# Performance work log

Hardware: AMD Instinct MI355X
Metric: run time of the kernel (lower is better)

Reference implementation:

```python
import jax, jax.numpy as jnp
import numpy as np
import math

B, N, D, H, T = 256, 512, 512, 8, 128
HD = D // H
CLIP = 10.0
CAP = 1.0
NEG = -1.0e9


def setup_inputs() -> dict:
    key = jax.random.key(0)
    ks = jax.random.split(key, 12)
    s = 1.0 / math.sqrt(D)
    return {
        "embeddings": jax.random.normal(ks[0], (B, N, D), jnp.float32),
        "mean_graph_emb": jax.random.normal(ks[1], (B, D), jnp.float32),
        "used_capacity": jax.random.uniform(ks[2], (T, B), jnp.float32),
        "Wk": jax.random.normal(ks[3], (D, D), jnp.float32) * s,
        "Wk_tanh": jax.random.normal(ks[4], (D, D), jnp.float32) * s,
        "Wv": jax.random.normal(ks[5], (D, D), jnp.float32) * s,
        "Wq_context": jax.random.normal(ks[6], (D, D), jnp.float32) * s,
        "Wq_step": jax.random.normal(ks[7], (D + 1, D), jnp.float32) * s,
        "Wout": jax.random.normal(ks[8], (D, D), jnp.float32) * s,
        "prev_a": jax.random.randint(ks[9], (T, B), 0, N, jnp.int32),
        "mask": jax.random.randint(ks[10], (T, B, N), 0, 2, jnp.int32),
    }


def reference(embeddings, mean_graph_emb, used_capacity, Wk, Wk_tanh, Wv,
              Wq_context, Wq_step, Wout, prev_a, mask):
    # Projections (done once per graph embedding, as in get_projections)
    K = (embeddings @ Wk).reshape(B, N, H, HD).transpose(0, 2, 1, 3)      # [B,H,N,hd]
    V = (embeddings @ Wv).reshape(B, N, H, HD).transpose(0, 2, 1, 3)      # [B,H,N,hd]
    K_tanh = embeddings @ Wk_tanh                                          # [B,N,D]
    Q_context = mean_graph_emb @ Wq_context                                # [B,D]

    inv_sqrt_hd = 1.0 / math.sqrt(HD)
    inv_sqrt_d = 1.0 / math.sqrt(D)

    def step(carry, xs):
        prev_t, cap_t, mask_t = xs  # [B], [B], [B,N]
        # get_step_context: gather prev node embedding + remaining capacity
        cur_emb = jnp.take_along_axis(embeddings, prev_t[:, None, None], axis=1)[:, 0]  # [B,D]
        step_ctx = jnp.concatenate([cur_emb, (CAP - cap_t)[:, None]], axis=-1)          # [B,D+1]
        q = Q_context + step_ctx @ Wq_step                                               # [B,D]
        qh = q.reshape(B, H, HD)                                                          # [B,H,hd]
        # decoder MHA, seq_len_q = 1
        logits = jnp.einsum("bhd,bhnd->bhn", qh, K) * inv_sqrt_hd                        # [B,H,N]
        logits = jnp.where(mask_t[:, None, :] == 1, NEG, logits)
        attn = jax.nn.softmax(logits, axis=-1)
        mha = jnp.einsum("bhn,bhnd->bhd", attn, V).reshape(B, D) @ Wout                  # [B,D]
        # single-head tanh-clipped pointer logits
        comp = jnp.einsum("bd,bnd->bn", mha, K_tanh) * inv_sqrt_d                        # [B,N]
        comp = jnp.tanh(comp) * CLIP
        comp = jnp.where(mask_t == 1, NEG, comp)
        p = jax.nn.softmax(comp, axis=-1)                                                # [B,N]
        return carry, p

    _, ps = jax.lax.scan(step, None, (prev_a, used_capacity, mask))  # [T,B,N]
    return ps.transpose(1, 0, 2)  # [B,T,N]
```

## Files before the change

kernel.cpp:

```cpp
#include <hip/hip_runtime.h>
#include <hip/hip_bf16.h>

constexpr int Bb = 256;
constexpr int Nn = 512;
constexpr int Dd = 512;
constexpr int Hh = 8;
constexpr int Tt = 128;
#define NEGF (-1.0e9f)

typedef __attribute__((ext_vector_type(4))) float f32x4;
typedef __attribute__((ext_vector_type(8))) short bf16x8;
typedef __attribute__((ext_vector_type(8))) unsigned short u16x8;

#define AS1 __attribute__((address_space(1)))
#define AS3 __attribute__((address_space(3)))

__device__ __forceinline__ unsigned short f2bf(float f) {
  union { float f; unsigned u; } v; v.f = f;
  unsigned r = v.u + 0x7fffu + ((v.u >> 16) & 1u);
  return (unsigned short)(r >> 16);
}

__device__ __forceinline__ unsigned cvtpk(float lo, float hi) {
  unsigned r;
  asm("v_cvt_pk_bf16_f32 %0, %1, %2" : "=v"(r) : "v"(lo), "v"(hi));
  return r;
}

__global__ void cast_emb_k(const float* __restrict__ src, unsigned short* __restrict__ dst, int n8) {
  int i = blockIdx.x * 256 + threadIdx.x;
  if (i >= n8) return;
  const float4* s = (const float4*)src + (size_t)i * 2;
  float4 a = s[0], b = s[1];
  u16x8 o;
  o[0] = f2bf(a.x); o[1] = f2bf(a.y); o[2] = f2bf(a.z); o[3] = f2bf(a.w);
  o[4] = f2bf(b.x); o[5] = f2bf(b.y); o[6] = f2bf(b.z); o[7] = f2bf(b.w);
  ((u16x8*)dst)[i] = o;
}

__global__ void cast_wt_k(const float* __restrict__ W0, const float* __restrict__ W1,
                          const float* __restrict__ W2,
                          unsigned short* __restrict__ D0, unsigned short* __restrict__ D1,
                          unsigned short* __restrict__ D2) {
  int mid = blockIdx.x >> 8;
  int tile = blockIdx.x & 255;
  const float* S = (mid == 0) ? W0 : (mid == 1) ? W1 : W2;
  unsigned short* Dst = (mid == 0) ? D0 : (mid == 1) ? D1 : D2;
  __shared__ float t[32][33];
  int r0 = (tile >> 4) * 32, c0 = (tile & 15) * 32;
  int tx = threadIdx.x & 31, ty = threadIdx.x >> 5;
#pragma unroll
  for (int yy = 0; yy < 4; ++yy) {
    int r = ty + yy * 8;
    t[r][tx] = S[(size_t)(r0 + r) * 512 + c0 + tx];
  }
  __syncthreads();
#pragma unroll
  for (int yy = 0; yy < 4; ++yy) {
    int c = ty + yy * 8;
    Dst[(size_t)(c0 + c) * 512 + r0 + tx] = f2bf(t[tx][c]);
  }
}

__global__ void qc_k(const float* __restrict__ mge, const float* __restrict__ Wqc,
                     float* __restrict__ Qc) {
  int b = blockIdx.x;
  __shared__ float m[512];
  m[threadIdx.x] = mge[(size_t)b * 512 + threadIdx.x];
  m[threadIdx.x + 256] = mge[(size_t)b * 512 + threadIdx.x + 256];
  __syncthreads();
  float a0 = 0.f, a1 = 0.f;
  for (int k = 0; k < 512; ++k) {
    float mk = m[k];
    a0 += mk * Wqc[(size_t)k * 512 + threadIdx.x];
    a1 += mk * Wqc[(size_t)k * 512 + threadIdx.x + 256];
  }
  Qc[(size_t)b * 512 + threadIdx.x] = a0;
  Qc[(size_t)b * 512 + threadIdx.x + 256] = a1;
}

__global__ void gather_k(const unsigned short* __restrict__ embB, const int* __restrict__ prev,
                         unsigned short* __restrict__ SC) {
  int row = blockIdx.x * 4 + (threadIdx.x >> 6);
  int lane = threadIdx.x & 63;
  int t = row >> 8, b = row & 255;
  int pa = prev[t * Bb + b];
  const u16x8* s = (const u16x8*)(embB + (size_t)(b * 512 + pa) * 512) + lane;
  *((u16x8*)(SC + (size_t)row * 512) + lane) = *s;
}

__global__ void mbits_k(const int* __restrict__ mask, unsigned* __restrict__ bits) {
  size_t gid = (size_t)blockIdx.x * 256 + threadIdx.x;
  int mv = mask[gid];
  unsigned long long bal = __ballot(mv == 1);
  if ((threadIdx.x & 63) == 0) {
    unsigned t = (unsigned)(gid >> 17);
    unsigned b = (unsigned)((gid >> 9) & 255);
    unsigned n = (unsigned)(gid & 511);
    unsigned* dst = bits + (((size_t)b * 128 + t) * 16 + (n >> 5));
    dst[0] = (unsigned)bal;
    dst[1] = (unsigned)(bal >> 32);
  }
}

__device__ __forceinline__ void stage_tile(const unsigned short* __restrict__ G, int row0, int k0,
                                           unsigned short* lds_base, int wave, int lane) {
#pragma unroll
  for (int c = 0; c < 4; ++c) {
    int chunk = wave * 4 + c;
    const unsigned short* g = G + (size_t)(row0 + chunk * 8 + (lane >> 3)) * 512 + k0 + (lane & 7) * 8;
    __builtin_amdgcn_global_load_lds((AS1 void*)g, (AS3 void*)(lds_base + chunk * 512), 16, 0, 0);
  }
}

template <int MODE>
__global__ __launch_bounds__(256, 2)
void gemm5_k(const unsigned short* __restrict__ A, const unsigned short* __restrict__ BT,
             void* __restrict__ Cout,
             const float* __restrict__ Qc, const float* __restrict__ WqsL,
             const float* __restrict__ capp) {
  __shared__ __align__(16) char lds[32768];
  unsigned short* ldsA = (unsigned short*)lds;
  unsigned short* ldsB = ldsA + 8192;
  int xcd = blockIdx.x & 7, loc = blockIdx.x >> 3;
  int ml = loc >> 2, nt = loc & 3;
  int mt = xcd * 32 + ml;
  int m0 = mt * 128, n0 = nt * 128;
  int tid = threadIdx.x, lane = tid & 63, w = tid >> 6;
  int wm = w >> 1, wn = w & 1;
  int l15 = lane & 15, l4 = lane >> 4;

  f32x4 acc[4][4] = {};
  for (int k0 = 0; k0 < 512; k0 += 64) {
    stage_tile(A, m0, k0, ldsA, w, lane);
    stage_tile(BT, n0, k0, ldsB, w, lane);
    __syncthreads();
#pragma unroll
    for (int ks = 0; ks < 2; ++ks) {
      bf16x8 fa[4], fb[4];
#pragma unroll
      for (int ii = 0; ii < 4; ++ii)
        fa[ii] = *(const bf16x8*)(ldsA + (wm * 64 + ii * 16 + l15) * 64 + ks * 32 + l4 * 8);
#pragma unroll
      for (int jj = 0; jj < 4; ++jj)
        fb[jj] = *(const bf16x8*)(ldsB + (wn * 64 + jj * 16 + l15) * 64 + ks * 32 + l4 * 8);
#pragma unroll
      for (int ii = 0; ii < 4; ++ii)
#pragma unroll
        for (int jj = 0; jj < 4; ++jj)
          acc[ii][jj] = __builtin_amdgcn_mfma_f32_16x16x32_bf16(fa[ii], fb[jj], acc[ii][jj], 0, 0, 0);
    }
    __syncthreads();
  }

  if (MODE == 1) {
    unsigned short* C = (unsigned short*)Cout;
#pragma unroll
    for (int ii = 0; ii < 4; ++ii)
#pragma unroll
      for (int jj = 0; jj < 4; ++jj)
#pragma unroll
        for (int r = 0; r < 4; ++r) {
          int row = m0 + wm * 64 + ii * 16 + l4 * 4 + r;
          int col = n0 + wn * 64 + jj * 16 + l15;
          C[(size_t)row * 512 + col] = f2bf(acc[ii][jj][r]);
        }
  } else {
    unsigned short* C = (unsigned short*)Cout;
#pragma unroll
    for (int ii = 0; ii < 4; ++ii)
#pragma unroll
      for (int jj = 0; jj < 4; ++jj)
#pragma unroll
        for (int r = 0; r < 4; ++r) {
          int row = m0 + wm * 64 + ii * 16 + l4 * 4 + r;
          int col = n0 + wn * 64 + jj * 16 + l15;
          int t = row >> 8, bbx = row & 255;
          float val = acc[ii][jj][r] + Qc[(size_t)bbx * 512 + col] + (1.0f - capp[row]) * WqsL[col];
          C[(size_t)(bbx * 128 + t) * 512 + col] = f2bf(val * 0.125f);
        }
  }
}

__global__ __launch_bounds__(256, 2)
void wf_k(const unsigned short* __restrict__ A, const unsigned short* __restrict__ BT,
          unsigned short* __restrict__ C) {
  __shared__ __align__(16) char lds[32768];
  unsigned short* ldsA = (unsigned short*)lds;
  unsigned short* ldsB = ldsA + 8192;
  int mt = blockIdx.x >> 2, nt = blockIdx.x & 3;
  int m0 = mt * 128, n0 = nt * 128;
  int tid = threadIdx.x, lane = tid & 63, w = tid >> 6;
  int wm = w >> 1, wn = w & 1;
  int l15 = lane & 15, l4 = lane >> 4;

  f32x4 acc[4][4] = {};
  for (int k0 = 0; k0 < 512; k0 += 64) {
    stage_tile(A, m0, k0, ldsA, w, lane);
    stage_tile(BT, n0, k0, ldsB, w, lane);
    __syncthreads();
#pragma unroll
    for (int ks = 0; ks < 2; ++ks) {
      bf16x8 fa[4], fb[4];
#pragma unroll
      for (int ii = 0; ii < 4; ++ii)
        fa[ii] = *(const bf16x8*)(ldsA + (wm * 64 + ii * 16 + l15) * 64 + ks * 32 + l4 * 8);
#pragma unroll
      for (int jj = 0; jj < 4; ++jj)
        fb[jj] = *(const bf16x8*)(ldsB + (wn * 64 + jj * 16 + l15) * 64 + ks * 32 + l4 * 8);
#pragma unroll
      for (int ii = 0; ii < 4; ++ii)
#pragma unroll
        for (int jj = 0; jj < 4; ++jj)
          acc[ii][jj] = __builtin_amdgcn_mfma_f32_16x16x32_bf16(fa[ii], fb[jj], acc[ii][jj], 0, 0, 0);
    }
    __syncthreads();
  }
#pragma unroll
  for (int ii = 0; ii < 4; ++ii)
#pragma unroll
    for (int jj = 0; jj < 4; ++jj)
#pragma unroll
      for (int r = 0; r < 4; ++r) {
        int row = m0 + wm * 64 + ii * 16 + l4 * 4 + r;
        int col = n0 + wn * 64 + jj * 16 + l15;
        C[(size_t)row * 512 + col] = f2bf(acc[ii][jj][r]);
      }
}

#define STAGE8(SLOT, MAT, H, KT)                                                   \
  do {                                                                             \
    const unsigned short* G_ = (MAT) ? BT : A;                                     \
    int rb_ = ((MAT) ? n0 : m0) + (H) * 128;                                       \
    char* Lb_ = lds + (SLOT) * 65536 + (MAT) * 32768 + (H) * 16384;                \
    _Pragma("unroll")                                                              \
    for (int sh_ = 0; sh_ < 2; ++sh_) {                                            \
      int off_ = sh_ * 8192 + tid * 16;                                            \
      int r_ = off_ >> 7;                                                          \
      int c_ = (off_ & 127) ^ ((r_ & 7) << 4);     \
      const char* g_ = (const char*)(G_ + (size_t)(rb_ + r_) * 512 + (KT) * 64) + c_; \
      __builtin_amdgcn_global_load_lds((AS1 void*)g_, (AS3 void*)(Lb_ + off_), 16, 0, 0); \
    }                                                                              \
  } while (0)

#define LDA_Q(QM)                                                   \
  _Pragma("unroll")                                                 \
  for (int ii = 0; ii < 4; ++ii) {                                  \
    int rr_ = (QM) * 64 + ii * 16 + l15;                            \
    const char* ap_ = ldsAh + rr_ * 128;                            \
    int sw_ = (rr_ & 7) << 4;                                       \
    fa[ii][0] = *(const bf16x8*)(ap_ + ((l4 * 16) ^ sw_));          \
    fa[ii][1] = *(const bf16x8*)(ap_ + ((64 + l4 * 16) ^ sw_));     \
  }

#define LDB_Q(QN)                                                   \
  _Pragma("unroll")                                                 \
  for (int jj = 0; jj < 2; ++jj) {                                  \
    int rr_ = (wn & 1) * 64 + (QN) * 32 + jj * 16 + l15;            \
    const char* bp_ = ldsBh + rr_ * 128;                            \
    int sw_ = (rr_ & 7) << 4;                                       \
    fb[jj][0] = *(const bf16x8*)(bp_ + ((l4 * 16) ^ sw_));          \
    fb[jj][1] = *(const bf16x8*)(bp_ + ((64 + l4 * 16) ^ sw_));     \
  }

#define MM16(QM, QN)                                                              \
  do {                                                                            \
    __builtin_amdgcn_s_setprio(1);                                                \
    _Pragma("unroll")                                                             \
    for (int ii = 0; ii < 4; ++ii)                                                \
      _Pragma("unroll")                                                           \
      for (int jj = 0; jj < 2; ++jj) {                                            \
        acc[(QM) * 4 + ii][(QN) * 2 + jj] = __builtin_amdgcn_mfma_f32_16x16x32_bf16( \
            fa[ii][0], fb[jj][0], acc[(QM) * 4 + ii][(QN) * 2 + jj], 0, 0, 0);    \
        acc[(QM) * 4 + ii][(QN) * 2 + jj] = __builtin_amdgcn_mfma_f32_16x16x32_bf16( \
            fa[ii][1], fb[jj][1], acc[(QM) * 4 + ii][(QN) * 2 + jj], 0, 0, 0);    \
      }                                                                           \
    __builtin_amdgcn_s_setprio(0);                                                \
  } while (0)

__global__ __launch_bounds__(512, 1)
void gemm8f_k(const unsigned short* __restrict__ A,
              const unsigned short* __restrict__ B0, const unsigned short* __restrict__ B1,
              unsigned short* __restrict__ C0, unsigned short* __restrict__ C2) {
  __shared__ __align__(16) char lds[131072];
  int xcd = blockIdx.x & 7, loc = blockIdx.x >> 3;
  int ml = loc >> 2, cmb = loc & 3;
  int grp = cmb >> 1, nh = cmb & 1;
  const unsigned short* BT = grp ? B1 : B0;
  int mt = xcd * 64 + ml;
  int m0 = mt * 256;
  int n0 = nh * 256;
  int tid = threadIdx.x, lane = tid & 63, w = tid >> 6;
  int wm = w >> 2, wn = w & 3;
  int l15 = lane & 15, l4 = lane >> 4;

  f32x4 acc[8][4] = {};
  bf16x8 fa[4][2], fb[2][2];

  STAGE8(0, 0, 0, 0); STAGE8(0, 0, 1, 0); STAGE8(0, 1, 0, 0); STAGE8(0, 1, 1, 0);

  for (int kt = 0; kt < 8; ++kt) {
    int s = kt & 1, sn = s ^ 1;
    char* ldsAh = lds + s * 65536 + wm * 16384;
    char* ldsBh = lds + s * 65536 + 32768 + (wn >> 1) * 16384;
    if (kt < 7) {
      STAGE8(sn, 0, 0, kt + 1);
      asm volatile("s_waitcnt vmcnt(2)" ::: "memory");
    } else {
      asm volatile("s_waitcnt vmcnt(0)" ::: "memory");
    }
    __builtin_amdgcn_s_barrier();
    LDA_Q(0); LDB_Q(0);
    MM16(0, 0);
    __builtin_amdgcn_s_barrier();
    LDB_Q(1);
    if (kt < 7) STAGE8(sn, 0, 1, kt + 1);
    __builtin_amdgcn_s_barrier();
    MM16(0, 1);
    __builtin_amdgcn_s_barrier();
    LDA_Q(1);
    if (kt < 7) STAGE8(sn, 1, 0, kt + 1);
    __builtin_amdgcn_s_barrier();
    MM16(1, 1);
    __builtin_amdgcn_s_barrier();
    LDB_Q(0);
    if (kt < 7) STAGE8(sn, 1, 1, kt + 1);
    __builtin_amdgcn_s_barrier();
    MM16(1, 0);
    __builtin_amdgcn_s_barrier();
  }

  if (grp == 0) {
#pragma unroll
    for (int mi = 0; mi < 8; ++mi)
#pragma unroll
      for (int nj = 0; nj < 4; ++nj)
#pragma unroll
        for (int r = 0; r < 4; ++r) {
          int row = m0 + wm * 128 + mi * 16 + l4 * 4 + r;
          int col = n0 + wn * 64 + nj * 16 + l15;
          C0[(size_t)row * 512 + col] = f2bf(acc[mi][nj][r]);
        }
  } else {
    int bb = m0 >> 9, nn0 = m0 & 511;
    char* wlds = lds + w * 16384;
#pragma unroll
    for (int p = 0; p < 2; ++p) {
#pragma unroll
      for (int njl = 0; njl < 2; ++njl) {
        int nj = p * 2 + njl;
#pragma unroll
        for (int mi = 0; mi < 8; ++mi) {
          ushort4 w4;
          w4.x = f2bf(acc[mi][nj][0]);
          w4.y = f2bf(acc[mi][nj][1]);
          w4.z = f2bf(acc[mi][nj][2]);
          w4.w = f2bf(acc[mi][nj][3]);
          int dc = njl * 16 + l15;
          int nl = mi * 16 + l4 * 4;
          *(ushort4*)(wlds + dc * 272 + nl * 2) = w4;
        }
      }
#pragma unroll
      for (int rr = 0; rr < 8; ++rr) {
        int dc = rr * 4 + l4;
        int n8 = l15 * 8;
        u16x8 v = *(const u16x8*)(wlds + dc * 272 + n8 * 2);
        int dglob = n0 + wn * 64 + p * 32 + dc;
        *(u16x8*)(C2 + (size_t)(bb * 512 + dglob) * 512 + nn0 + wm * 128 + n8) = v;
      }
    }
  }
}

#define STAGEK5(CH, SLOT)                                                          \
  do {                                                                             \
    _Pragma("unroll")                                                              \
    for (int sh_ = 0; sh_ < 2; ++sh_) {                                            \
      int off_ = sh_ * 8192 + tid * 16;                                            \
      int r_ = off_ >> 7;                                                          \
      int c_ = (off_ & 127) ^ ((r_ & 7) << 4);                                     \
      const char* g_ = (const char*)(Kb + (size_t)(b * 512 + (CH) * 128 + r_) * 512 + h * 64) + c_; \
      __builtin_amdgcn_global_load_lds((AS1 void*)g_, (AS3 void*)(lds + (SLOT) * 16384 + off_), 16, 0, 0); \
    }                                                                              \
  } while (0)

#define STAGEV5(CH, SLOT)                                                          \
  do {                                                                             \
    _Pragma("unroll")                                                              \
    for (int sh_ = 0; sh_ < 2; ++sh_) {                                            \
      int off_ = sh_ * 8192 + tid * 16;                                            \
      int r_ = off_ >> 8;                                                          \
      int c_ = (off_ & 255) ^ ((r_ & 7) << 4);                                     \
      const char* g_ = (const char*)(Vt + (size_t)(b * 512 + h * 64 + r_) * 512 + (CH) * 128) + c_; \
      __builtin_amdgcn_global_load_lds((AS1 void*)g_, (AS3 void*)(lds + 32768 + (SLOT) * 16384 + off_), 16, 0, 0); \
    }                                                                              \
  } while (0)

#define CHUNK5(CH)                                                                 \
  do {                                                                             \
    const char* Ks_ = lds + ((CH) & 1) * 16384;                                    \
    const char* Vs_ = lds + 32768 + ((CH) & 1) * 16384;                            \
    f32x4 sck[8];                                                                  \
    _Pragma("unroll")                                                              \
    for (int jj = 0; jj < 8; ++jj) sck[jj] = (f32x4){0.f, 0.f, 0.f, 0.f};          \
    _Pragma("unroll")                                                              \
    for (int jj = 0; jj < 8; ++jj) {                                               \
      int rr_ = jj * 16 + l15;                                                     \
      int sw_ = (rr_ & 7) << 4;                                                    \
      bf16x8 k0_ = *(const bf16x8*)(Ks_ + rr_ * 128 + ((l4 * 16) ^ sw_));          \
      bf16x8 k1_ = *(const bf16x8*)(Ks_ + rr_ * 128 + ((64 + l4 * 16) ^ sw_));     \
      sck[jj] = __builtin_amdgcn_mfma_f32_16x16x32_bf16(k0_, fq[0], sck[jj], 0, 0, 0); \
      sck[jj] = __builtin_amdgcn_mfma_f32_16x16x32_bf16(k1_, fq[1], sck[jj], 0, 0, 0); \
    }                                                                              \
    unsigned mwarr_[4] = {mqs[CH].x, mqs[CH].y, mqs[CH].z, mqs[CH].w};             \
    float cmx_ = -3.0e38f;                                                         \
    _Pragma("unroll")                                                              \
    for (int jj = 0; jj < 8; ++jj) {                                               \
      unsigned nib_ = mwarr_[jj >> 1] >> (((jj & 1) << 4) + (l4 << 2));            \
      _Pragma("unroll")                                                            \
      for (int r = 0; r < 4; ++r)                                                  \
        sck[jj][r] = ((nib_ >> r) & 1) ? NEGF : sck[jj][r];                        \
      float m01_ = fmaxf(sck[jj][0], sck[jj][1]);                                  \
      float m23_ = fmaxf(sck[jj][2], sck[jj][3]);                                  \
      cmx_ = fmaxf(cmx_, fmaxf(m01_, m23_));                                       \
    }                                                                              \
    cmx_ = fmaxf(cmx_, __shfl_xor(cmx_, 16));                                      \
    cmx_ = fmaxf(cmx_, __shfl_xor(cmx_, 32));                                      \
    float mn_ = fmaxf(mx, cmx_);                                                   \
    float al_ = __expf(mx - mn_);                                                  \
    sum *= al_;                                                                    \
    _Pragma("unroll")                                                              \
    for (int dj = 0; dj < 4; ++dj)                                                 \
      _Pragma("unroll")                                                            \
      for (int r = 0; r < 4; ++r) o[dj][r] *= al_;                                 \
    mx = mn_;                                                                      \
    _Pragma("unroll")                                                              \
    for (int jj = 0; jj < 8; ++jj) {                                               \
      _Pragma("unroll")                                                            \
      for (int r = 0; r < 4; ++r) sck[jj][r] = __expf(sck[jj][r] - mx);            \
      sum += (sck[jj][0] + sck[jj][1]) + (sck[jj][2] + sck[jj][3]);                \
    }                                                                              \
    _Pragma("unroll")                                                              \
    for (int g = 0; g < 4; ++g) {                                                  \
      unsigned a0_ = cvtpk(sck[2 * g][0], sck[2 * g][1]);                          \
      unsigned a1_ = cvtpk(sck[2 * g][2], sck[2 * g][3]);                          \
      unsigned b0_ = cvtpk(sck[2 * g + 1][0], sck[2 * g + 1][1]);                  \
      unsigned b1_ = cvtpk(sck[2 * g + 1][2], sck[2 * g + 1][3]);                  \
      unsigned wA0_ = __shfl(a0_, src0, 64), wB0_ = __shfl(b0_, src0, 64);         \
      unsigned wA1_ = __shfl(a1_, src0, 64), wB1_ = __shfl(b1_, src0, 64);         \
      unsigned wA2_ = __shfl(a0_, src2, 64), wB2_ = __shfl(b0_, src2, 64);         \
      unsigned wA3_ = __shfl(a1_, src2, 64), wB3_ = __shfl(b1_, src2, 64);         \
      union { unsigned u[4]; bf16x8 v; } pu_;                                      \
      pu_.u[0] = loh ? wA0_ : wB0_;                                                \
      pu_.u[1] = loh ? wA1_ : wB1_;                                                \
      pu_.u[2] = loh ? wA2_ : wB2_;                                                \
      pu_.u[3] = loh ? wA3_ : wB3_;                                                \
      _Pragma("unroll")                                                            \
      for (int dj = 0; dj < 4; ++dj) {                                             \
        int rr_ = dj * 16 + l15;                                                   \
        int sw_ = (rr_ & 7) << 4;                                                  \
        bf16x8 fv_ = *(const bf16x8*)(Vs_ + rr_ * 256 + ((g * 64 + l4 * 16) ^ sw_)); \
        o[dj] = __builtin_amdgcn_mfma_f32_16x16x32_bf16(fv_, pu_.v, o[dj], 0, 0, 0); \
      }                                                                            \
    }                                                                              \
  } while (0)

__global__ __launch_bounds__(512, 4)
void attn5_k(const unsigned short* __restrict__ Qb, const unsigned short* __restrict__ Kb,
             const unsigned short* __restrict__ Vt, const unsigned* __restrict__ mbits,
             unsigned short* __restrict__ mhaB) {
  __shared__ __align__(16) char lds[65536];
  int bid = blockIdx.x;
  int h = bid & 7, b = bid >> 3;
  int tid = threadIdx.x, lane = tid & 63, w = tid >> 6;
  int l15 = lane & 15, l4 = lane >> 4;
  int t = w * 16 + l15;

  bf16x8 fq[2];
#pragma unroll
  for (int ks = 0; ks < 2; ++ks)
    fq[ks] = *(const bf16x8*)(Qb + (size_t)(b * 128 + t) * 512 + h * 64 + ks * 32 + l4 * 8);
  uint4 mqs[4];
  {
    const uint4* mp = (const uint4*)(mbits + (((size_t)b * 128 + t) << 4));
    mqs[0] = mp[0]; mqs[1] = mp[1]; mqs[2] = mp[2]; mqs[3] = mp[3];
  }

  float mx = -3.0e38f, sum = 0.f;
  f32x4 o[4] = {};
  int src0 = l15 + ((l4 & 1) ? 32 : 0);
  int src2 = l15 + ((l4 & 1) ? 48 : 16);
  bool loh = (l4 < 2);

  STAGEK5(0, 0); STAGEV5(0, 0);
  STAGEK5(1, 1); STAGEV5(1, 1);
  asm volatile("s_waitcnt vmcnt(4)" ::: "memory");
  __builtin_amdgcn_s_barrier();
  CHUNK5(0);
  __builtin_amdgcn_s_barrier();
  STAGEK5(2, 0); STAGEV5(2, 0);
  asm volatile("s_waitcnt vmcnt(4)" ::: "memory");
  __builtin_amdgcn_s_barrier();
  CHUNK5(1);
  __builtin_amdgcn_s_barrier();
  STAGEK5(3, 1); STAGEV5(3, 1);
  asm volatile("s_waitcnt vmcnt(4)" ::: "memory");
  __builtin_amdgcn_s_barrier();
  CHUNK5(2);
  __builtin_amdgcn_s_barrier();
  asm volatile("s_waitcnt vmcnt(0)" ::: "memory");
  __builtin_amdgcn_s_barrier();
  CHUNK5(3);

  sum += __shfl_xor(sum, 16);
  sum += __shfl_xor(sum, 32);
  float inv = 1.0f / sum;
#pragma unroll
  for (int dj = 0; dj < 4; ++dj) {
    ushort4 w4;
    w4.x = f2bf(o[dj][0] * inv);
    w4.y = f2bf(o[dj][1] * inv);
    w4.z = f2bf(o[dj][2] * inv);
    w4.w = f2bf(o[dj][3] * inv);
    *(ushort4*)(mhaB + (size_t)(b * 128 + t) * 512 + h * 64 + dj * 16 + l4 * 4) = w4;
  }
}

#define STAGEC(CH, SLOT)                                                           \
  do {                                                                             \
    _Pragma("unroll")                                                              \
    for (int ps_ = 0; ps_ < 8; ++ps_) {                                            \
      int off_ = ps_ * 8192 + tid * 16;                                            \
      int r_ = off_ >> 10;                                                         \
      int c_ = (off_ & 1023) ^ ((r_ & 7) << 4);                                    \
      const char* g_ = (const char*)(embB + (size_t)(b * 512 + (CH) * 64 + r_) * 512) + c_; \
      __builtin_amdgcn_global_load_lds((AS1 void*)g_, (AS3 void*)(lds + (SLOT) * 65536 + off_), 16, 0, 0); \
    }                                                                              \
  } while (0)

#define CCHUNK(CH)                                                                 \
  do {                                                                             \
    const char* Es_ = lds + ((CH) & 1) * 65536;                                    \
    _Pragma("unroll")                                                              \
    for (int jjl_ = 0; jjl_ < 4; ++jjl_) {                                         \
      f32x4 sck = (f32x4){0.f, 0.f, 0.f, 0.f};                                     \
      int rr_ = jjl_ * 16 + l15;                                                   \
      const char* ep_ = Es_ + rr_ * 1024;                                          \
      int sw_ = (rr_ & 7) << 4;                                                    \
      _Pragma("unroll")                                                            \
      for (int ks_ = 0; ks_ < 16; ++ks_) {                                         \
        bf16x8 fa_ = *(const bf16x8*)(ep_ + ((ks_ * 64 + l4 * 16) ^ sw_));         \
        sck = __builtin_amdgcn_mfma_f32_16x16x32_bf16(fa_, fb[ks_], sck, 0, 0, 0); \
      }                                                                            \
      int jg_ = (CH) * 4 + jjl_;                                                   \
      unsigned nib_ = mw[jg_ >> 1] >> (((jg_ & 1) << 4) + (l4 << 2));              \
      float4 o4_;                                                                  \
      float* po_ = (float*)&o4_;                                                   \
      _Pragma("unroll")                                                            \
      for (int r = 0; r < 4; ++r) {                                                \
        float y_ = sck[r] * 0.044194173824159216f;                                 \
        y_ = fminf(fmaxf(y_, -15.f), 15.f);                                        \
        float e2_ = __expf(2.f * y_);                                              \
        float th_ = (e2_ - 1.f) / (e2_ + 1.f);                                     \
        float p_ = __expf(th_ * 10.f - 10.f);                                      \
        p_ = ((nib_ >> r) & 1) ? 0.f : p_;                                         \
        po_[r] = p_;                                                               \
        sum += p_;                                                                 \
      }                                                                            \
      *(float4*)(out + (size_t)(b * 128 + t) * 512 + (CH) * 64 + jjl_ * 16 + l4 * 4) = o4_; \
    }                                                                              \
  } while (0)

__global__ __launch_bounds__(512, 1)
void comp4_k(const unsigned short* __restrict__ mh2, const unsigned short* __restrict__ embB,
             const unsigned* __restrict__ mbits, float* __restrict__ out,
             float* __restrict__ sums) {
  __shared__ __align__(16) char lds[131072];
  int b = blockIdx.x;
  int tid = threadIdx.x, lane = tid & 63, w = tid >> 6;
  int l15 = lane & 15, l4 = lane >> 4;
  int t = w * 16 + l15;

  bf16x8 fb[16];
#pragma unroll
  for (int ks = 0; ks < 16; ++ks)
    fb[ks] = *(const bf16x8*)(mh2 + (size_t)(b * 128 + t) * 512 + ks * 32 + l4 * 8);
  unsigned mw[16];
  {
    const uint4* mp = (const uint4*)(mbits + (((size_t)b * 128 + t) << 4));
    uint4 a0 = mp[0], a1 = mp[1], a2 = mp[2], a3 = mp[3];
    mw[0] = a0.x; mw[1] = a0.y; mw[2] = a0.z; mw[3] = a0.w;
    mw[4] = a1.x; mw[5] = a1.y; mw[6] = a1.z; mw[7] = a1.w;
    mw[8] = a2.x; mw[9] = a2.y; mw[10] = a2.z; mw[11] = a2.w;
    mw[12] = a3.x; mw[13] = a3.y; mw[14] = a3.z; mw[15] = a3.w;
  }

  float sum = 0.f;
  STAGEC(0, 0);
  STAGEC(1, 1);
  asm volatile("s_waitcnt vmcnt(8)" ::: "memory");
  __builtin_amdgcn_s_barrier();
  CCHUNK(0);
  __builtin_amdgcn_s_barrier();
  STAGEC(2, 0);
  asm volatile("s_waitcnt vmcnt(8)" ::: "memory");
  __builtin_amdgcn_s_barrier();
  CCHUNK(1);
  __builtin_amdgcn_s_barrier();
  STAGEC(3, 1);
  asm volatile("s_waitcnt vmcnt(8)" ::: "memory");
  __builtin_amdgcn_s_barrier();
  CCHUNK(2);
  __builtin_amdgcn_s_barrier();
  STAGEC(4, 0);
  asm volatile("s_waitcnt vmcnt(8)" ::: "memory");
  __builtin_amdgcn_s_barrier();
  CCHUNK(3);
  __builtin_amdgcn_s_barrier();
  STAGEC(5, 1);
  asm volatile("s_waitcnt vmcnt(8)" ::: "memory");
  __builtin_amdgcn_s_barrier();
  CCHUNK(4);
  __builtin_amdgcn_s_barrier();
  STAGEC(6, 0);
  asm volatile("s_waitcnt vmcnt(8)" ::: "memory");
  __builtin_amdgcn_s_barrier();
  CCHUNK(5);
  __builtin_amdgcn_s_barrier();
  STAGEC(7, 1);
  asm volatile("s_waitcnt vmcnt(8)" ::: "memory");
  __builtin_amdgcn_s_barrier();
  CCHUNK(6);
  __builtin_amdgcn_s_barrier();
  asm volatile("s_waitcnt vmcnt(0)" ::: "memory");
  __builtin_amdgcn_s_barrier();
  CCHUNK(7);

  sum += __shfl_xor(sum, 16);
  sum += __shfl_xor(sum, 32);
  if (l4 == 0) sums[b * 128 + t] = sum;
}

__global__ void norm_k(float* __restrict__ out, const float* __restrict__ sums) {
  int row = blockIdx.x * 4 + (threadIdx.x >> 6);
  int lane = threadIdx.x & 63;
  float inv = 1.0f / sums[row];
  float4* p = (float4*)(out + (size_t)row * 512) + lane;
  float4 a = p[0], b = p[64];
  a.x *= inv; a.y *= inv; a.z *= inv; a.w *= inv;
  b.x *= inv; b.y *= inv; b.z *= inv; b.w *= inv;
  p[0] = a; p[64] = b;
}

extern "C" void kernel_launch(void* const* d_in, const int* in_sizes, int n_in,
                              void* d_out, int out_size, void* d_ws, size_t ws_size,
                              hipStream_t stream) {
  (void)in_sizes; (void)n_in; (void)out_size; (void)ws_size;
  const float* emb  = (const float*)d_in[0];
  const float* mge  = (const float*)d_in[1];
  const float* cap  = (const float*)d_in[2];
  const float* Wk   = (const float*)d_in[3];
  const float* Wkt  = (const float*)d_in[4];
  const float* Wv   = (const float*)d_in[5];
  const float* Wqc  = (const float*)d_in[6];
  const float* Wqs  = (const float*)d_in[7];
  const float* Wout = (const float*)d_in[8];
  const int* prev   = (const int*)d_in[9];
  const int* mask   = (const int*)d_in[10];
  float* out = (float*)d_out;

  char* p = (char*)d_ws;
  auto take = [&](size_t n) { char* q = p; p += (n + 255) & ~(size_t)255; return q; };
  unsigned short* embB = (unsigned short*)take((size_t)131072 * 512 * 2);
  unsigned short* Kb   = (unsigned short*)take((size_t)131072 * 512 * 2);
  unsigned short* Vt   = (unsigned short*)take((size_t)131072 * 512 * 2);
  unsigned short* SCe  = (unsigned short*)take((size_t)32768 * 512 * 2);
  unsigned short* Qb   = (unsigned short*)take((size_t)32768 * 512 * 2);
  unsigned short* mhaB = (unsigned short*)take((size_t)32768 * 512 * 2);
  unsigned short* mh2  = (unsigned short*)take((size_t)32768 * 512 * 2);
  float*          Qc   = (float*)take((size_t)256 * 512 * 4);
  unsigned*       mbit = (unsigned*)take((size_t)256 * 128 * 16 * 4);
  float*          sums = (float*)take((size_t)32768 * 4);
  unsigned short* WkT  = (unsigned short*)take(524288);
  unsigned short* WvT  = (unsigned short*)take(524288);
  unsigned short* WqsT = (unsigned short*)take(524288);
  unsigned short* WktB = (unsigned short*)take(524288);
  unsigned short* WoutB= (unsigned short*)take(524288);
  unsigned short* WFT  = (unsigned short*)take(524288);

  cast_emb_k<<<32768, 256, 0, stream>>>(emb, embB, 8388608);
  cast_emb_k<<<128, 256, 0, stream>>>(Wkt, WktB, 32768);
  cast_emb_k<<<128, 256, 0, stream>>>(Wout, WoutB, 32768);
  cast_wt_k<<<768, 256, 0, stream>>>(Wk, Wv, Wqs, WkT, WvT, WqsT);
  qc_k<<<256, 256, 0, stream>>>(mge, Wqc, Qc);
  gather_k<<<8192, 256, 0, stream>>>(embB, prev, SCe);
  mbits_k<<<65536, 256, 0, stream>>>(mask, mbit);
  wf_k<<<16, 256, 0, stream>>>(WktB, WoutB, WFT);
  gemm5_k<3><<<1024, 256, 0, stream>>>(SCe, WqsT, Qb, Qc, Wqs + 512 * 512, cap);
  gemm8f_k<<<2048, 512, 0, stream>>>(embB, WkT, WvT, Kb, Vt);
  attn5_k<<<2048, 512, 0, stream>>>(Qb, Kb, Vt, mbit, mhaB);
  gemm5_k<1><<<1024, 256, 0, stream>>>(mhaB, WFT, mh2, nullptr, nullptr, nullptr);
  comp4_k<<<256, 512, 0, stream>>>(mh2, embB, mbit, out, sums);
  norm_k<<<8192, 256, 0, stream>>>(out, sums);
}
```

Measured before the change: 556.5 us.

## Make K/V projection GEMM process four M-tiles per block with cross-tile prefetch

The fused K/V projection GEMM now loops over four consecutive 256-row M tiles inside one block, and the grid drops from 2048 to 512 blocks. The next tile's first K-slice is prefetched during the last K-step of the current tile, so global-to-LDS loads overlap each tile's epilogue and prologue. The transpose epilogue now uses the idle LDS buffer with a smaller per-wave staging area. The aim is to cut per-block launch, prologue and pipeline-drain overhead. The cost is fewer blocks for load balancing, plus an extra barrier and an accumulator reset per tile.

Measured after the change: 548.8 us. No clear change (-1.4%).

```diff
diff --git a/kernel.cpp b/kernel.cpp
--- a/kernel.cpp
+++ b/kernel.cpp
@@ -228,10 +228,10 @@
       }
 }
 
-#define STAGE8(SLOT, MAT, H, KT)                                                   \
+#define STAGE10(SLOT, MAT, H, ROWB, KT)                                            \
   do {                                                                             \
     const unsigned short* G_ = (MAT) ? BT : A;                                     \
-    int rb_ = ((MAT) ? n0 : m0) + (H) * 128;                                       \
+    int rb_ = (ROWB) + (H) * 128;                                                  \
     char* Lb_ = lds + (SLOT) * 65536 + (MAT) * 32768 + (H) * 16384;                \
     _Pragma("unroll")                                                              \
     for (int sh_ = 0; sh_ < 2; ++sh_) {                                            \
@@ -279,16 +279,15 @@
   } while (0)
 
 __global__ __launch_bounds__(512, 1)
-void gemm8f_k(const unsigned short* __restrict__ A,
+void gemm10_k(const unsigned short* __restrict__ A,
               const unsigned short* __restrict__ B0, const unsigned short* __restrict__ B1,
               unsigned short* __restrict__ C0, unsigned short* __restrict__ C2) {
   __shared__ __align__(16) char lds[131072];
   int xcd = blockIdx.x & 7, loc = blockIdx.x >> 3;
-  int ml = loc >> 2, cmb = loc & 3;
+  int ml4 = loc >> 2, cmb = loc & 3;
   int grp = cmb >> 1, nh = cmb & 1;
   const unsigned short* BT = grp ? B1 : B0;
-  int mt = xcd * 64 + ml;
-  int m0 = mt * 256;
+  int mtb = xcd * 64 + ml4 * 4;
   int n0 = nh * 256;
   int tid = threadIdx.x, lane = tid & 63, w = tid >> 6;
   int wm = w >> 2, wn = w & 3;
@@ -297,14 +296,21 @@
   f32x4 acc[8][4] = {};
   bf16x8 fa[4][2], fb[2][2];
 
-  STAGE8(0, 0, 0, 0); STAGE8(0, 0, 1, 0); STAGE8(0, 1, 0, 0); STAGE8(0, 1, 1, 0);
-
-  for (int kt = 0; kt < 8; ++kt) {
-    int s = kt & 1, sn = s ^ 1;
+  {
+    int m0n = mtb * 256;
+    STAGE10(0, 0, 0, m0n, 0); STAGE10(0, 0, 1, m0n, 0);
+    STAGE10(0, 1, 0, n0, 0);  STAGE10(0, 1, 1, n0, 0);
+  }
+
+  for (int g = 0; g < 32; ++g) {
+    int s = g & 1, sn = s ^ 1;
     char* ldsAh = lds + s * 65536 + wm * 16384;
     char* ldsBh = lds + s * 65536 + 32768 + (wn >> 1) * 16384;
-    if (kt < 7) {
-      STAGE8(sn, 0, 0, kt + 1);
+    int gn = g + 1;
+    int m0n = (mtb + (gn >> 3)) * 256;
+    int ktn = gn & 7;
+    if (g < 31) {
+      STAGE10(sn, 0, 0, m0n, ktn);
       asm volatile("s_waitcnt vmcnt(2)" ::: "memory");
     } else {
       asm volatile("s_waitcnt vmcnt(0)" ::: "memory");
@@ -314,61 +320,65 @@
     MM16(0, 0);
     __builtin_amdgcn_s_barrier();
     LDB_Q(1);
-    if (kt < 7) STAGE8(sn, 0, 1, kt + 1);
+    if (g < 31) STAGE10(sn, 0, 1, m0n, ktn);
     __builtin_amdgcn_s_barrier();
     MM16(0, 1);
     __builtin_amdgcn_s_barrier();
     LDA_Q(1);
-    if (kt < 7) STAGE8(sn, 1, 0, kt + 1);
+    if (g < 31) STAGE10(sn, 1, 0, n0, ktn);
     __builtin_amdgcn_s_barrier();
     MM16(1, 1);
     __builtin_amdgcn_s_barrier();
     LDB_Q(0);
-    if (kt < 7) STAGE8(sn, 1, 1, kt + 1);
+    if (g < 31) STAGE10(sn, 1, 1, n0, ktn);
     __builtin_amdgcn_s_barrier();
     MM16(1, 0);
     __builtin_amdgcn_s_barrier();
-  }
-
-  if (grp == 0) {
-#pragma unroll
-    for (int mi = 0; mi < 8; ++mi)
-#pragma unroll
-      for (int nj = 0; nj < 4; ++nj)
-#pragma unroll
-        for (int r = 0; r < 4; ++r) {
-          int row = m0 + wm * 128 + mi * 16 + l4 * 4 + r;
-          int col = n0 + wn * 64 + nj * 16 + l15;
-          C0[(size_t)row * 512 + col] = f2bf(acc[mi][nj][r]);
-        }
-  } else {
-    int bb = m0 >> 9, nn0 = m0 & 511;
-    char* wlds = lds + w * 16384;
-#pragma unroll
-    for (int p = 0; p < 2; ++p) {
-#pragma unroll
-      for (int njl = 0; njl < 2; ++njl) {
-        int nj = p * 2 + njl;
-#pragma unroll
-        for (int mi = 0; mi < 8; ++mi) {
-          ushort4 w4;
-          w4.x = f2bf(acc[mi][nj][0]);
-          w4.y = f2bf(acc[mi][nj][1]);
-          w4.z = f2bf(acc[mi][nj][2]);
-          w4.w = f2bf(acc[mi][nj][3]);
-          int dc = njl * 16 + l15;
-          int nl = mi * 16 + l4 * 4;
-          *(ushort4*)(wlds + dc * 272 + nl * 2) = w4;
+
+    if ((g & 7) == 7) {
+      int m0cur = (mtb + (g >> 3)) * 256;
+      if (grp == 0) {
+#pragma unroll
+        for (int mi = 0; mi < 8; ++mi)
+#pragma unroll
+          for (int nj = 0; nj < 4; ++nj)
+#pragma unroll
+            for (int r = 0; r < 4; ++r) {
+              int row = m0cur + wm * 128 + mi * 16 + l4 * 4 + r;
+              int col = n0 + wn * 64 + nj * 16 + l15;
+              C0[(size_t)row * 512 + col] = f2bf(acc[mi][nj][r]);
+            }
+      } else {
+        int bb = m0cur >> 9, nn0 = m0cur & 511;
+        char* wb = lds + 65536 + w * 8192;
+#pragma unroll
+        for (int p = 0; p < 4; ++p) {
+#pragma unroll
+          for (int mi = 0; mi < 8; ++mi) {
+            ushort4 w4;
+            w4.x = f2bf(acc[mi][p][0]);
+            w4.y = f2bf(acc[mi][p][1]);
+            w4.z = f2bf(acc[mi][p][2]);
+            w4.w = f2bf(acc[mi][p][3]);
+            *(ushort4*)(wb + l15 * 264 + (mi * 16 + l4 * 4) * 2) = w4;
+          }
+#pragma unroll
+          for (int step = 0; step < 4; ++step) {
+            int dl = step * 4 + l4;
+            union { ushort4 h[2]; u16x8 v; } u;
+            u.h[0] = *(const ushort4*)(wb + dl * 264 + l15 * 16);
+            u.h[1] = *(const ushort4*)(wb + dl * 264 + l15 * 16 + 8);
+            int dglob = n0 + wn * 64 + p * 16 + dl;
+            *(u16x8*)(C2 + (size_t)(bb * 512 + dglob) * 512 + nn0 + wm * 128 + l15 * 8) = u.v;
+          }
         }
       }
 #pragma unroll
-      for (int rr = 0; rr < 8; ++rr) {
-        int dc = rr * 4 + l4;
-        int n8 = l15 * 8;
-        u16x8 v = *(const u16x8*)(wlds + dc * 272 + n8 * 2);
-        int dglob = n0 + wn * 64 + p * 32 + dc;
-        *(u16x8*)(C2 + (size_t)(bb * 512 + dglob) * 512 + nn0 + wm * 128 + n8) = v;
-      }
+      for (int mi = 0; mi < 8; ++mi)
+#pragma unroll
+        for (int nj = 0; nj < 4; ++nj)
+          acc[mi][nj] = (f32x4){0.f, 0.f, 0.f, 0.f};
+      __syncthreads();
     }
   }
 }
@@ -698,7 +708,7 @@
   mbits_k<<<65536, 256, 0, stream>>>(mask, mbit);
   wf_k<<<16, 256, 0, stream>>>(WktB, WoutB, WFT);
   gemm5_k<3><<<1024, 256, 0, stream>>>(SCe, WqsT, Qb, Qc, Wqs + 512 * 512, cap);
-  gemm8f_k<<<2048, 512, 0, stream>>>(embB, WkT, WvT, Kb, Vt);
+  gemm10_k<<<512, 512, 0, stream>>>(embB, WkT, WvT, Kb, Vt);
   attn5_k<<<2048, 512, 0, stream>>>(Qb, Kb, Vt, mbit, mhaB);
   gemm5_k<1><<<1024, 256, 0, stream>>>(mhaB, WFT, mh2, nullptr, nullptr, nullptr);
   comp4_k<<<256, 512, 0, stream>>>(mh2, embB, mbit, out, sums);
```
